# Kernel tuning notes

Hardware: AMD Instinct MI355X
Metric: run time of the kernel (lower is better)

## Reference

```python
import jax, jax.numpy as jnp
import numpy as np

B, T, E = 32, 2048, 1024

def setup_inputs() -> dict:
    key = jax.random.key(0)
    k1, k2, k3 = jax.random.split(key, 3)
    enc = jax.random.normal(k1, (B, T, E), dtype=jnp.float32)
    ctx = jax.random.normal(k2, (B, E), dtype=jnp.float32)
    W = jax.random.normal(k3, (E, E), dtype=jnp.float32) * 0.05
    b = jnp.zeros((1, E), dtype=jnp.float32)
    return {"enc": enc, "ctx": ctx, "W": W, "b": b}

def reference(enc, ctx, W, b):
    # ht: (B, T, E) = tanh(enc @ W + b)
    ht = jnp.tanh(jnp.einsum('bte,ef->btf', enc, W) + b)
    # scores: (B, T) = batch dot of ctx against each timestep of ht
    scores = jnp.einsum('be,bte->bt', ctx, ht)
    at = jax.nn.softmax(scores, axis=-1)
    # weighted sum pooling over time -> (B, E)
    return jnp.einsum('bt,bte->be', at, ht)
```

## Files before the change

### kernel.cpp

```cpp
#include <hip/hip_runtime.h>
#include <hip/hip_bf16.h>
#include <math.h>

typedef unsigned short u16;
typedef unsigned int   u32;
typedef short bf16x8 __attribute__((ext_vector_type(8)));
typedef float f32x4  __attribute__((ext_vector_type(4)));

#define Bb 32
#define Tt 2048
#define Ee 1024
#define Mm (Bb*Tt)
#define LSTR 40

__device__ __forceinline__ float tanh_fast(float x) {
  float ax = fminf(fabsf(x), 15.0f);
  float e  = __expf(2.0f * ax);
  float t  = 1.0f - 2.0f / (e + 1.0f);
  return copysignf(t, x);
}

__device__ __forceinline__ void cvt2(float a0, float a1, u32& hi, u32& lo) {
  u32 u0 = __float_as_uint(a0), u1 = __float_as_uint(a1);
  hi = (u0 >> 16) | (u1 & 0xffff0000u);
  float r0 = a0 - __uint_as_float(u0 & 0xffff0000u);
  float r1 = a1 - __uint_as_float(u1 & 0xffff0000u);
  lo = (__float_as_uint(r0) >> 16) | (__float_as_uint(r1) & 0xffff0000u);
}

__global__ __launch_bounds__(256) void wt_convert(const float* __restrict__ W,
                                                  u16* __restrict__ Wt_hi,
                                                  u16* __restrict__ Wt_lo) {
  __shared__ float tile[32][33];
  int n0 = blockIdx.x * 32, k0 = blockIdx.y * 32;
  int tx = threadIdx.x, ty = threadIdx.y;
#pragma unroll
  for (int i = 0; i < 4; ++i)
    tile[ty + 8*i][tx] = W[(size_t)(k0 + ty + 8*i) * Ee + n0 + tx];
  __syncthreads();
#pragma unroll
  for (int i = 0; i < 4; ++i) {
    float v = tile[tx][ty + 8*i];
    u32 u = __float_as_uint(v);
    u16 hi = (u16)(u >> 16);
    float rem = v - __uint_as_float(u & 0xffff0000u);
    u16 lo = (u16)(__float_as_uint(rem) >> 16);
    size_t idx = (size_t)(n0 + ty + 8*i) * Ee + k0 + tx;
    Wt_hi[idx] = hi;
    Wt_lo[idx] = lo;
  }
}

__global__ __launch_bounds__(256, 2) void gemm_tanh_score(
    const float* __restrict__ enc, const float* __restrict__ ctx,
    const float* __restrict__ bias,
    const u16* __restrict__ Wt_hi, const u16* __restrict__ Wt_lo,
    u16* __restrict__ ht, float* __restrict__ scores) {
  __shared__ u16 Ahi[128*LSTR], Alo[128*LSTR], Bhi[128*LSTR], Blo[128*LSTR];

  int bx = blockIdx.x;
  int nt = bx & 7, mt = bx >> 3;
  int m0 = mt * 128, n0 = nt * 128;
  int tid = threadIdx.x;
  int w = tid >> 6, lane = tid & 63;
  int wm = (w & 1) * 64, wn = (w >> 1) * 64;
  int q = lane >> 4, c = lane & 15;

  f32x4 zero = {0.f, 0.f, 0.f, 0.f};
  f32x4 acc[4][4];
#pragma unroll
  for (int i = 0; i < 4; ++i)
#pragma unroll
    for (int j = 0; j < 4; ++j) acc[i][j] = zero;

  int ar = tid >> 1, ah = tid & 1;
  const float* Ap  = enc   + (size_t)(m0 + ar) * Ee + ah * 16;
  const u16*   BhP = Wt_hi + (size_t)(n0 + ar) * Ee + ah * 16;
  const u16*   BlP = Wt_lo + (size_t)(n0 + ar) * Ee + ah * 16;
  u16* AhiW = &Ahi[ar * LSTR + ah * 16];
  u16* AloW = &Alo[ar * LSTR + ah * 16];
  u16* BhiW = &Bhi[ar * LSTR + ah * 16];
  u16* BloW = &Blo[ar * LSTR + ah * 16];

  for (int kt = 0; kt < 32; ++kt) {
    const float4* ap = (const float4*)(Ap + (size_t)kt * 32);
    float4 f0 = ap[0], f1 = ap[1], f2 = ap[2], f3 = ap[3];
    const uint4* bhp = (const uint4*)(BhP + (size_t)kt * 32);
    uint4 bH0 = bhp[0], bH1 = bhp[1];
    const uint4* blp = (const uint4*)(BlP + (size_t)kt * 32);
    uint4 bL0 = blp[0], bL1 = blp[1];

    u32 hi[8], lo[8];
    cvt2(f0.x, f0.y, hi[0], lo[0]); cvt2(f0.z, f0.w, hi[1], lo[1]);
    cvt2(f1.x, f1.y, hi[2], lo[2]); cvt2(f1.z, f1.w, hi[3], lo[3]);
    cvt2(f2.x, f2.y, hi[4], lo[4]); cvt2(f2.z, f2.w, hi[5], lo[5]);
    cvt2(f3.x, f3.y, hi[6], lo[6]); cvt2(f3.z, f3.w, hi[7], lo[7]);

    __syncthreads();
    ((uint4*)AhiW)[0] = make_uint4(hi[0], hi[1], hi[2], hi[3]);
    ((uint4*)AhiW)[1] = make_uint4(hi[4], hi[5], hi[6], hi[7]);
    ((uint4*)AloW)[0] = make_uint4(lo[0], lo[1], lo[2], lo[3]);
    ((uint4*)AloW)[1] = make_uint4(lo[4], lo[5], lo[6], lo[7]);
    ((uint4*)BhiW)[0] = bH0; ((uint4*)BhiW)[1] = bH1;
    ((uint4*)BloW)[0] = bL0; ((uint4*)BloW)[1] = bL1;
    __syncthreads();

    bf16x8 aH[4], aL[4], bH[4], bL[4];
#pragma unroll
    for (int i = 0; i < 4; ++i) {
      int rax = (wm + i * 16 + c) * LSTR + q * 8;
      aH[i] = *(const bf16x8*)(&Ahi[rax]);
      aL[i] = *(const bf16x8*)(&Alo[rax]);
      int rbx = (wn + i * 16 + c) * LSTR + q * 8;
      bH[i] = *(const bf16x8*)(&Bhi[rbx]);
      bL[i] = *(const bf16x8*)(&Blo[rbx]);
    }
#pragma unroll
    for (int i = 0; i < 4; ++i)
#pragma unroll
      for (int j = 0; j < 4; ++j) {
        acc[i][j] = __builtin_amdgcn_mfma_f32_16x16x32_bf16(aH[i], bH[j], acc[i][j], 0, 0, 0);
        acc[i][j] = __builtin_amdgcn_mfma_f32_16x16x32_bf16(aH[i], bL[j], acc[i][j], 0, 0, 0);
        acc[i][j] = __builtin_amdgcn_mfma_f32_16x16x32_bf16(aL[i], bH[j], acc[i][j], 0, 0, 0);
      }
  }

  int bidx = m0 >> 11;
  float ctxv[4], biasv[4];
#pragma unroll
  for (int j = 0; j < 4; ++j) {
    int col = n0 + wn + j * 16 + c;
    ctxv[j]  = ctx[bidx * Ee + col];
    biasv[j] = bias[col];
  }
#pragma unroll
  for (int i = 0; i < 4; ++i) {
#pragma unroll
    for (int r = 0; r < 4; ++r) {
      int rowG = m0 + wm + i * 16 + q * 4 + r;
      u16* hrow = ht + (size_t)rowG * Ee + n0 + wn + c;
      float s = 0.f;
#pragma unroll
      for (int j = 0; j < 4; ++j) {
        float h = tanh_fast(acc[i][j][r] + biasv[j]);
        __hip_bfloat16 hb = __float2bfloat16(h);
        hrow[j * 16] = *(u16*)&hb;
        s += h * ctxv[j];
      }
      s += __shfl_xor(s, 1); s += __shfl_xor(s, 2);
      s += __shfl_xor(s, 4); s += __shfl_xor(s, 8);
      if (c == 0) atomicAdd(&scores[rowG], s);
    }
  }
}

__global__ __launch_bounds__(256) void softmax_t(const float* __restrict__ scores,
                                                 float* __restrict__ at) {
  __shared__ float red[256];
  int b = blockIdx.x, tid = threadIdx.x;
  float v[8];
  float mx = -3.0e38f;
#pragma unroll
  for (int i = 0; i < 8; ++i) {
    v[i] = scores[b * Tt + i * 256 + tid];
    mx = fmaxf(mx, v[i]);
  }
  red[tid] = mx; __syncthreads();
  for (int s = 128; s > 0; s >>= 1) {
    if (tid < s) red[tid] = fmaxf(red[tid], red[tid + s]);
    __syncthreads();
  }
  mx = red[0]; __syncthreads();
  float sum = 0.f;
#pragma unroll
  for (int i = 0; i < 8; ++i) { v[i] = __expf(v[i] - mx); sum += v[i]; }
  red[tid] = sum; __syncthreads();
  for (int s = 128; s > 0; s >>= 1) {
    if (tid < s) red[tid] += red[tid + s];
    __syncthreads();
  }
  float inv = 1.0f / red[0];
#pragma unroll
  for (int i = 0; i < 8; ++i) at[b * Tt + i * 256 + tid] = v[i] * inv;
}

__global__ __launch_bounds__(256) void weighted_sum(const u16* __restrict__ ht,
                                                    const float* __restrict__ at,
                                                    float* __restrict__ out) {
  __shared__ float ats[512];
  int bx = blockIdx.x;
  int b = bx >> 3, sub = bx & 7, ec = sub & 1, tc = sub >> 1;
  for (int i = threadIdx.x; i < 512; i += 256) ats[i] = at[b * Tt + tc * 512 + i];
  __syncthreads();
  int e = ec * 512 + threadIdx.x * 2;
  const u16* base = ht + (size_t)(b * Tt + tc * 512) * Ee + e;
  float s0 = 0.f, s1 = 0.f;
  for (int tt = 0; tt < 512; ++tt) {
    float a = ats[tt];
    u32 u = *(const u32*)(base + (size_t)tt * Ee);
    s0 += a * __uint_as_float(u << 16);
    s1 += a * __uint_as_float(u & 0xffff0000u);
  }
  atomicAdd(&out[b * Ee + e], s0);
  atomicAdd(&out[b * Ee + e + 1], s1);
}

extern "C" void kernel_launch(void* const* d_in, const int* in_sizes, int n_in,
                              void* d_out, int out_size, void* d_ws, size_t ws_size,
                              hipStream_t stream) {
  const float* enc  = (const float*)d_in[0];
  const float* ctx  = (const float*)d_in[1];
  const float* W    = (const float*)d_in[2];
  const float* bias = (const float*)d_in[3];
  float* out = (float*)d_out;

  char* ws = (char*)d_ws;
  u16* Wt_hi = (u16*)(ws);
  u16* Wt_lo = (u16*)(ws + (size_t)2 * 1024 * 1024);
  u16* ht    = (u16*)(ws + (size_t)4 * 1024 * 1024);
  float* scores = (float*)(ws + (size_t)4 * 1024 * 1024 + (size_t)Mm * Ee * 2);
  float* at     = scores + Mm;

  hipMemsetAsync(scores, 0, (size_t)Mm * sizeof(float), stream);
  hipMemsetAsync(out, 0, (size_t)Bb * Ee * sizeof(float), stream);

  wt_convert<<<dim3(32, 32), dim3(32, 8), 0, stream>>>(W, Wt_hi, Wt_lo);
  gemm_tanh_score<<<dim3(4096), dim3(256), 0, stream>>>(enc, ctx, bias, Wt_hi, Wt_lo, ht, scores);
  softmax_t<<<dim3(32), dim3(256), 0, stream>>>(scores, at);
  weighted_sum<<<dim3(256), dim3(256), 0, stream>>>(ht, at, out);
}
```

Baseline: 771.7 us.

## Use fp16 two-term split GEMM and atomic-free partial weighted sum

Replaces the three-MFMA bf16 hi/lo split with an fp16 scheme: the activation is rounded to a single fp16 and only the weight keeps a hi/lo split, so two MFMAs per tile. This removes one MFMA per tile and the low-part shared buffer. The weighted sum now writes per-chunk partials into reused workspace and a small reduce kernel sums them, replacing atomics. Casting activations to fp16 lowers their precision and risks overflow for large-magnitude inputs.

Result: faster. 716.5 us (-7.2%).

```diff
diff --git a/kernel.cpp b/kernel.cpp
--- a/kernel.cpp
+++ b/kernel.cpp
@@ -4,7 +4,7 @@
 
 typedef unsigned short u16;
 typedef unsigned int   u32;
-typedef short bf16x8 __attribute__((ext_vector_type(8)));
+typedef _Float16 f16x8 __attribute__((ext_vector_type(8)));
 typedef float f32x4  __attribute__((ext_vector_type(4)));
 
 #define Bb 32
@@ -20,12 +20,9 @@
   return copysignf(t, x);
 }
 
-__device__ __forceinline__ void cvt2(float a0, float a1, u32& hi, u32& lo) {
-  u32 u0 = __float_as_uint(a0), u1 = __float_as_uint(a1);
-  hi = (u0 >> 16) | (u1 & 0xffff0000u);
-  float r0 = a0 - __uint_as_float(u0 & 0xffff0000u);
-  float r1 = a1 - __uint_as_float(u1 & 0xffff0000u);
-  lo = (__float_as_uint(r0) >> 16) | (__float_as_uint(r1) & 0xffff0000u);
+__device__ __forceinline__ u32 pack2h(float a, float b) {
+  _Float16 ha = (_Float16)a, hb = (_Float16)b;
+  return (u32)__builtin_bit_cast(u16, ha) | ((u32)__builtin_bit_cast(u16, hb) << 16);
 }
 
 __global__ __launch_bounds__(256) void wt_convert(const float* __restrict__ W,
@@ -41,13 +38,12 @@
 #pragma unroll
   for (int i = 0; i < 4; ++i) {
     float v = tile[tx][ty + 8*i];
-    u32 u = __float_as_uint(v);
-    u16 hi = (u16)(u >> 16);
-    float rem = v - __uint_as_float(u & 0xffff0000u);
-    u16 lo = (u16)(__float_as_uint(rem) >> 16);
+    _Float16 hi = (_Float16)v;
+    float rem = v - (float)hi;
+    _Float16 lo = (_Float16)rem;
     size_t idx = (size_t)(n0 + ty + 8*i) * Ee + k0 + tx;
-    Wt_hi[idx] = hi;
-    Wt_lo[idx] = lo;
+    Wt_hi[idx] = __builtin_bit_cast(u16, hi);
+    Wt_lo[idx] = __builtin_bit_cast(u16, lo);
   }
 }
 
@@ -56,7 +52,7 @@
     const float* __restrict__ bias,
     const u16* __restrict__ Wt_hi, const u16* __restrict__ Wt_lo,
     u16* __restrict__ ht, float* __restrict__ scores) {
-  __shared__ u16 Ahi[128*LSTR], Alo[128*LSTR], Bhi[128*LSTR], Blo[128*LSTR];
+  __shared__ u16 Ahf[128*LSTR], Bhi[128*LSTR], Blo[128*LSTR];
 
   int bx = blockIdx.x;
   int nt = bx & 7, mt = bx >> 3;
@@ -77,10 +73,9 @@
   const float* Ap  = enc   + (size_t)(m0 + ar) * Ee + ah * 16;
   const u16*   BhP = Wt_hi + (size_t)(n0 + ar) * Ee + ah * 16;
   const u16*   BlP = Wt_lo + (size_t)(n0 + ar) * Ee + ah * 16;
-  u16* AhiW = &Ahi[ar * LSTR + ah * 16];
-  u16* AloW = &Alo[ar * LSTR + ah * 16];
-  u16* BhiW = &Bhi[ar * LSTR + ah * 16];
-  u16* BloW = &Blo[ar * LSTR + ah * 16];
+  u16* AW  = &Ahf[ar * LSTR + ah * 16];
+  u16* BhW = &Bhi[ar * LSTR + ah * 16];
+  u16* BlW = &Blo[ar * LSTR + ah * 16];
 
   for (int kt = 0; kt < 32; ++kt) {
     const float4* ap = (const float4*)(Ap + (size_t)kt * 32);
@@ -90,38 +85,33 @@
     const uint4* blp = (const uint4*)(BlP + (size_t)kt * 32);
     uint4 bL0 = blp[0], bL1 = blp[1];
 
-    u32 hi[8], lo[8];
-    cvt2(f0.x, f0.y, hi[0], lo[0]); cvt2(f0.z, f0.w, hi[1], lo[1]);
-    cvt2(f1.x, f1.y, hi[2], lo[2]); cvt2(f1.z, f1.w, hi[3], lo[3]);
-    cvt2(f2.x, f2.y, hi[4], lo[4]); cvt2(f2.z, f2.w, hi[5], lo[5]);
-    cvt2(f3.x, f3.y, hi[6], lo[6]); cvt2(f3.z, f3.w, hi[7], lo[7]);
-
-    __syncthreads();
-    ((uint4*)AhiW)[0] = make_uint4(hi[0], hi[1], hi[2], hi[3]);
-    ((uint4*)AhiW)[1] = make_uint4(hi[4], hi[5], hi[6], hi[7]);
-    ((uint4*)AloW)[0] = make_uint4(lo[0], lo[1], lo[2], lo[3]);
-    ((uint4*)AloW)[1] = make_uint4(lo[4], lo[5], lo[6], lo[7]);
-    ((uint4*)BhiW)[0] = bH0; ((uint4*)BhiW)[1] = bH1;
-    ((uint4*)BloW)[0] = bL0; ((uint4*)BloW)[1] = bL1;
-    __syncthreads();
-
-    bf16x8 aH[4], aL[4], bH[4], bL[4];
+    u32 a01 = pack2h(f0.x, f0.y), a23 = pack2h(f0.z, f0.w);
+    u32 a45 = pack2h(f1.x, f1.y), a67 = pack2h(f1.z, f1.w);
+    u32 a89 = pack2h(f2.x, f2.y), aAB = pack2h(f2.z, f2.w);
+    u32 aCD = pack2h(f3.x, f3.y), aEF = pack2h(f3.z, f3.w);
+
+    __syncthreads();
+    ((uint4*)AW)[0]  = make_uint4(a01, a23, a45, a67);
+    ((uint4*)AW)[1]  = make_uint4(a89, aAB, aCD, aEF);
+    ((uint4*)BhW)[0] = bH0; ((uint4*)BhW)[1] = bH1;
+    ((uint4*)BlW)[0] = bL0; ((uint4*)BlW)[1] = bL1;
+    __syncthreads();
+
+    f16x8 aF[4], bH[4], bL[4];
 #pragma unroll
     for (int i = 0; i < 4; ++i) {
       int rax = (wm + i * 16 + c) * LSTR + q * 8;
-      aH[i] = *(const bf16x8*)(&Ahi[rax]);
-      aL[i] = *(const bf16x8*)(&Alo[rax]);
+      aF[i] = *(const f16x8*)(&Ahf[rax]);
       int rbx = (wn + i * 16 + c) * LSTR + q * 8;
-      bH[i] = *(const bf16x8*)(&Bhi[rbx]);
-      bL[i] = *(const bf16x8*)(&Blo[rbx]);
+      bH[i] = *(const f16x8*)(&Bhi[rbx]);
+      bL[i] = *(const f16x8*)(&Blo[rbx]);
     }
 #pragma unroll
     for (int i = 0; i < 4; ++i)
 #pragma unroll
       for (int j = 0; j < 4; ++j) {
-        acc[i][j] = __builtin_amdgcn_mfma_f32_16x16x32_bf16(aH[i], bH[j], acc[i][j], 0, 0, 0);
-        acc[i][j] = __builtin_amdgcn_mfma_f32_16x16x32_bf16(aH[i], bL[j], acc[i][j], 0, 0, 0);
-        acc[i][j] = __builtin_amdgcn_mfma_f32_16x16x32_bf16(aL[i], bH[j], acc[i][j], 0, 0, 0);
+        acc[i][j] = __builtin_amdgcn_mfma_f32_16x16x32_f16(aF[i], bH[j], acc[i][j], 0, 0, 0);
+        acc[i][j] = __builtin_amdgcn_mfma_f32_16x16x32_f16(aF[i], bL[j], acc[i][j], 0, 0, 0);
       }
   }
 
@@ -186,23 +176,39 @@
 
 __global__ __launch_bounds__(256) void weighted_sum(const u16* __restrict__ ht,
                                                     const float* __restrict__ at,
-                                                    float* __restrict__ out) {
-  __shared__ float ats[512];
+                                                    float* __restrict__ part) {
+  __shared__ float ats[64];
   int bx = blockIdx.x;
-  int b = bx >> 3, sub = bx & 7, ec = sub & 1, tc = sub >> 1;
-  for (int i = threadIdx.x; i < 512; i += 256) ats[i] = at[b * Tt + tc * 512 + i];
+  int b = bx >> 5, tc = bx & 31;
+  int tid = threadIdx.x;
+  if (tid < 64) ats[tid] = at[b * Tt + tc * 64 + tid];
   __syncthreads();
-  int e = ec * 512 + threadIdx.x * 2;
-  const u16* base = ht + (size_t)(b * Tt + tc * 512) * Ee + e;
-  float s0 = 0.f, s1 = 0.f;
-  for (int tt = 0; tt < 512; ++tt) {
-    float a = ats[tt];
-    u32 u = *(const u32*)(base + (size_t)tt * Ee);
-    s0 += a * __uint_as_float(u << 16);
-    s1 += a * __uint_as_float(u & 0xffff0000u);
-  }
-  atomicAdd(&out[b * Ee + e], s0);
-  atomicAdd(&out[b * Ee + e + 1], s1);
+  int e0 = tid * 4;
+  const u16* base = ht + (size_t)(b * Tt + tc * 64) * Ee + e0;
+  float s0 = 0.f, s1 = 0.f, s2 = 0.f, s3 = 0.f;
+#pragma unroll 4
+  for (int t = 0; t < 64; ++t) {
+    float a = ats[t];
+    uint2 u = *(const uint2*)(base + (size_t)t * Ee);
+    s0 += a * __uint_as_float(u.x << 16);
+    s1 += a * __uint_as_float(u.x & 0xffff0000u);
+    s2 += a * __uint_as_float(u.y << 16);
+    s3 += a * __uint_as_float(u.y & 0xffff0000u);
+  }
+  float4 out4 = make_float4(s0, s1, s2, s3);
+  *(float4*)(part + ((size_t)(b * 32 + tc) * Ee + e0)) = out4;
+}
+
+__global__ __launch_bounds__(256) void reduce_part(const float* __restrict__ part,
+                                                   float* __restrict__ out) {
+  int b = blockIdx.x, tid = threadIdx.x;
+  float4 s = make_float4(0.f, 0.f, 0.f, 0.f);
+#pragma unroll
+  for (int tc = 0; tc < 32; ++tc) {
+    float4 p = ((const float4*)(part + (size_t)(b * 32 + tc) * Ee))[tid];
+    s.x += p.x; s.y += p.y; s.z += p.z; s.w += p.w;
+  }
+  ((float4*)(out + (size_t)b * Ee))[tid] = s;
 }
 
 extern "C" void kernel_launch(void* const* d_in, const int* in_sizes, int n_in,
@@ -220,12 +226,13 @@
   u16* ht    = (u16*)(ws + (size_t)4 * 1024 * 1024);
   float* scores = (float*)(ws + (size_t)4 * 1024 * 1024 + (size_t)Mm * Ee * 2);
   float* at     = scores + Mm;
+  float* part   = (float*)ws;
 
   hipMemsetAsync(scores, 0, (size_t)Mm * sizeof(float), stream);
-  hipMemsetAsync(out, 0, (size_t)Bb * Ee * sizeof(float), stream);
 
   wt_convert<<<dim3(32, 32), dim3(32, 8), 0, stream>>>(W, Wt_hi, Wt_lo);
   gemm_tanh_score<<<dim3(4096), dim3(256), 0, stream>>>(enc, ctx, bias, Wt_hi, Wt_lo, ht, scores);
   softmax_t<<<dim3(32), dim3(256), 0, stream>>>(scores, at);
-  weighted_sum<<<dim3(256), dim3(256), 0, stream>>>(ht, at, out);
-}
+  weighted_sum<<<dim3(1024), dim3(256), 0, stream>>>(ht, at, part);
+  reduce_part<<<dim3(32), dim3(256), 0, stream>>>(part, out);
+}
```
